# Kernel optimization log

Measured on AMD Instinct MI355X. Metric: run time of the kernel, lower is better.

Reference implementation:

```python
import jax, jax.numpy as jnp
import numpy as np

B, L, D = 4, 4096, 2048
E = 64           # num_experts
K = 2            # top_k
AUX_W = 0.01     # aux_loss_weight


def setup_inputs() -> dict:
    key = jax.random.key(0)
    kx, kw = jax.random.split(key)
    x = jax.random.normal(kx, (B, L, D), dtype=jnp.float32)
    W = jax.random.normal(kw, (E, D), dtype=jnp.float32) * 0.02  # nn.init.normal_(std=0.02)
    return {"x": x, "W": W}


def reference(x, W):
    # gate: logits [B, L, E]
    logits = jnp.einsum('bld,ed->ble', x, W)
    # full softmax over experts (used for aux loss)
    probs = jax.nn.softmax(logits, axis=-1)
    # top-k selection and renormalized weights
    top_k_logits, top_k_indices = jax.lax.top_k(logits, K)      # [B, L, K]
    top_k_weights = jax.nn.softmax(top_k_logits, axis=-1)       # [B, L, K]
    # load-balance aux loss (Switch-style): uses top-1 expert assignment
    expert_mask = jax.nn.one_hot(top_k_indices[..., 0], E, dtype=jnp.float32)  # [B, L, E]
    expert_fraction = expert_mask.mean(axis=(0, 1))              # [E]
    prob_fraction = probs.mean(axis=(0, 1))                      # [E]
    aux_loss = E * jnp.sum(expert_fraction * prob_fraction) * AUX_W
    return top_k_indices, top_k_weights, aux_loss
```

## Files before the change

### kernel.cpp

```cpp
#include <hip/hip_runtime.h>

#define D_DIM 2048
#define E_NUM 64
#define M_TOK 16384
#define BK 32
#define XS_ROW 33
#define XS_TILE (64 * XS_ROW)


__global__ __launch_bounds__(128) void init_kernel(float* __restrict__ g) {
    g[threadIdx.x] = 0.0f;
}

__global__ __launch_bounds__(256) void wt_kernel(const float* __restrict__ W,
                                                 float* __restrict__ Wt) {
    const int i4 = blockIdx.x * 256 + threadIdx.x;
    const int e  = i4 >> 9;
    const int k4 = (i4 & 511) << 2;
    const float4 v = *(const float4*)&W[e * D_DIM + k4];
    Wt[(k4 + 0) * E_NUM + e] = v.x;
    Wt[(k4 + 1) * E_NUM + e] = v.y;
    Wt[(k4 + 2) * E_NUM + e] = v.z;
    Wt[(k4 + 3) * E_NUM + e] = v.w;
}

__global__ __launch_bounds__(512, 1) void fused_kernel(
    const float* __restrict__ x, const float* __restrict__ Wt,
    float* __restrict__ out, float* __restrict__ gprob, float* __restrict__ gcnt)
{
    __shared__ float lds[4 * XS_TILE];

    const int tid  = threadIdx.x;
    const int wid  = tid >> 6;
    const int lane = tid & 63;
    const int h    = wid >> 2;
    const int eb   = (wid & 3) << 4;
    const long tok0 = (long)blockIdx.x * 64;
    const int ku = __builtin_amdgcn_readfirstlane((wid >> 2) << 10);
    const int eu = __builtin_amdgcn_readfirstlane((wid & 3) << 4);

    const int sh   = tid >> 8;
    const int ss   = tid & 255;
    const int srow = ss >> 2;
    const int sc   = (ss & 3) << 2;
    const float* xsrc = x + (tok0 + srow) * D_DIM + (sh << 10) + sc;

    double accd[16];
    #pragma unroll
    for (int e = 0; e < 16; ++e) accd[e] = 0.0;

    float4 v0 = *(const float4*)(xsrc);
    float4 v1 = *(const float4*)(xsrc + 16);
    {
        float* d = lds + (sh * 2) * XS_TILE + srow * XS_ROW + sc;
        d[0] = v0.x; d[1] = v0.y; d[2] = v0.z; d[3] = v0.w;
        d[16] = v1.x; d[17] = v1.y; d[18] = v1.z; d[19] = v1.w;
    }
    __syncthreads();

    for (int it = 0; it < 32; ++it) {
        if (it < 31) {
            const float* p = xsrc + (it + 1) * BK;
            v0 = *(const float4*)(p);
            v1 = *(const float4*)(p + 16);
        }
        const float* xb = lds + (h * 2 + (it & 1)) * XS_TILE + lane * XS_ROW;
        const int kb0 = ku + it * BK;
        #pragma unroll 1
        for (int c2 = 0; c2 < 2; ++c2) {
            float accc[16];
            #pragma unroll
            for (int e = 0; e < 16; ++e) accc[e] = 0.0f;
            const float* xc = xb + c2 * 16;
            const float* wp = Wt + (size_t)(kb0 + c2 * 16) * E_NUM + eu;
            #pragma unroll 1
            for (int q = 0; q < 4; ++q) {
                const float xr[4] = { xc[q * 4 + 0], xc[q * 4 + 1],
                                      xc[q * 4 + 2], xc[q * 4 + 3] };
                float4 w0[4], w1[4], w2[4], w3[4];
                #pragma unroll
                for (int k2 = 0; k2 < 4; ++k2) {
                    const float* wr = wp + (q * 4 + k2) * E_NUM;
                    w0[k2] = *(const float4*)(wr + 0);
                    w1[k2] = *(const float4*)(wr + 4);
                    w2[k2] = *(const float4*)(wr + 8);
                    w3[k2] = *(const float4*)(wr + 12);
                }
                #pragma unroll
                for (int k2 = 0; k2 < 4; ++k2) {
                    const float xk = xr[k2];
                    accc[0]  += xk * w0[k2].x;  accc[1]  += xk * w0[k2].y;
                    accc[2]  += xk * w0[k2].z;  accc[3]  += xk * w0[k2].w;
                    accc[4]  += xk * w1[k2].x;  accc[5]  += xk * w1[k2].y;
                    accc[6]  += xk * w1[k2].z;  accc[7]  += xk * w1[k2].w;
                    accc[8]  += xk * w2[k2].x;  accc[9]  += xk * w2[k2].y;
                    accc[10] += xk * w2[k2].z;  accc[11] += xk * w2[k2].w;
                    accc[12] += xk * w3[k2].x;  accc[13] += xk * w3[k2].y;
                    accc[14] += xk * w3[k2].z;  accc[15] += xk * w3[k2].w;
                }
            }
            #pragma unroll
            for (int e = 0; e < 16; ++e) accd[e] += (double)accc[e];
        }
        if (it < 31) {
            float* d = lds + (sh * 2 + ((it + 1) & 1)) * XS_TILE + srow * XS_ROW + sc;
            d[0] = v0.x; d[1] = v0.y; d[2] = v0.z; d[3] = v0.w;
            d[16] = v1.x; d[17] = v1.y; d[18] = v1.z; d[19] = v1.w;
        }
        __syncthreads();
    }

    {
        float* sp = lds + h * 4096 + lane * 64 + eb;
        *(float4*)(sp + 0)  = make_float4((float)accd[0],  (float)accd[1],
                                          (float)accd[2],  (float)accd[3]);
        *(float4*)(sp + 4)  = make_float4((float)accd[4],  (float)accd[5],
                                          (float)accd[6],  (float)accd[7]);
        *(float4*)(sp + 8)  = make_float4((float)accd[8],  (float)accd[9],
                                          (float)accd[10], (float)accd[11]);
        *(float4*)(sp + 12) = make_float4((float)accd[12], (float)accd[13],
                                          (float)accd[14], (float)accd[15]);
    }
    __syncthreads();

    float pacc = 0.0f, cacc = 0.0f;
    if (h == 0) {
        const int q = wid & 3;
        for (int i = 0; i < 16; ++i) {
            const int  tl = q * 16 + i;
            const long t  = tok0 + tl;
            const float l = lds[tl * 64 + lane] + lds[4096 + tl * 64 + lane];
            float m1 = l; int i1 = lane;
            #pragma unroll
            for (int off = 32; off > 0; off >>= 1) {
                const float ov = __shfl_xor(m1, off, 64);
                const int   oi = __shfl_xor(i1, off, 64);
                if (ov > m1 || (ov == m1 && oi < i1)) { m1 = ov; i1 = oi; }
            }
            const float p = __expf(l - m1);
            float s = p;
            #pragma unroll
            for (int off = 32; off > 0; off >>= 1) s += __shfl_xor(s, off, 64);
            pacc += p / s;
            if (lane == i1) cacc += 1.0f;
            const float lm = (lane == i1) ? -1e30f : l;
            float m2 = lm; int i2 = lane;
            #pragma unroll
            for (int off = 32; off > 0; off >>= 1) {
                const float ov = __shfl_xor(m2, off, 64);
                const int   oi = __shfl_xor(i2, off, 64);
                if (ov > m2 || (ov == m2 && oi < i2)) { m2 = ov; i2 = oi; }
            }
            if (lane == 0) {
                out[2 * t]     = (float)i1;
                out[2 * t + 1] = (float)i2;
                const float w1 = 1.0f / (1.0f + __expf(m2 - m1));
                out[2 * M_TOK + 2 * t]     = w1;
                out[2 * M_TOK + 2 * t + 1] = 1.0f - w1;
            }
        }
    }
    __syncthreads();
    if (h == 0) {
        lds[(wid & 3) * 64 + lane]       = pacc;
        lds[256 + (wid & 3) * 64 + lane] = cacc;
    }
    __syncthreads();
    if (wid == 0) {
        atomicAdd(&gprob[lane], lds[lane] + lds[64 + lane] + lds[128 + lane] + lds[192 + lane]);
        atomicAdd(&gcnt[lane],  lds[256 + lane] + lds[320 + lane] + lds[384 + lane] + lds[448 + lane]);
    }
}

__global__ __launch_bounds__(64) void aux_kernel(
    const float* __restrict__ gprob, const float* __restrict__ gcnt,
    float* __restrict__ out)
{
    const int lane = threadIdx.x;
    float v = gprob[lane] * gcnt[lane];
    #pragma unroll
    for (int off = 32; off > 0; off >>= 1) v += __shfl_xor(v, off, 64);
    if (lane == 0)
        out[4 * M_TOK] = 64.0f * 0.01f * v / ((float)M_TOK * (float)M_TOK);
}

extern "C" void kernel_launch(void* const* d_in, const int* in_sizes, int n_in,
                              void* d_out, int out_size, void* d_ws, size_t ws_size,
                              hipStream_t stream)
{
    const float* x = (const float*)d_in[0];
    const float* W = (const float*)d_in[1];
    float* out   = (float*)d_out;
    float* gprob = (float*)d_ws;
    float* gcnt  = gprob + 64;
    float* Wt    = gprob + 128;

    init_kernel<<<1, 128, 0, stream>>>(gprob);
    wt_kernel<<<128, 256, 0, stream>>>(W, Wt);
    fused_kernel<<<256, 512, 0, stream>>>(x, Wt, out, gprob, gcnt);
    aux_kernel<<<1, 64, 0, stream>>>(gprob, gcnt, out);
}
```

Baseline: 293.1 us.

## Double wavefronts per block, halve experts per wave, fold init into transpose kernel

Blocks grow from 512 to 1024 threads, so each wavefront accumulates 8 experts instead of 16. The x staging rows are padded to 36 so shared-memory reads and writes can use float4. This is meant to raise latency hiding and cut register pressure on the single-block-per-CU grid of 256 blocks. The zero-initialisation kernel is merged into the weight transpose kernel to save one launch. Each W row now gets loaded by twice as many waves in total, and the top-k epilogue still runs on only 4 of the 16 waves.

```diff
diff --git a/kernel.cpp b/kernel.cpp
--- a/kernel.cpp
+++ b/kernel.cpp
@@ -4,16 +4,14 @@
 #define E_NUM 64
 #define M_TOK 16384
 #define BK 32
-#define XS_ROW 33
+#define XS_ROW 36
 #define XS_TILE (64 * XS_ROW)
 
 
-__global__ __launch_bounds__(128) void init_kernel(float* __restrict__ g) {
-    g[threadIdx.x] = 0.0f;
-}
-
 __global__ __launch_bounds__(256) void wt_kernel(const float* __restrict__ W,
-                                                 float* __restrict__ Wt) {
+                                                 float* __restrict__ Wt,
+                                                 float* __restrict__ g) {
+    if (blockIdx.x == 0 && threadIdx.x < 128) g[threadIdx.x] = 0.0f;
     const int i4 = blockIdx.x * 256 + threadIdx.x;
     const int e  = i4 >> 9;
     const int k4 = (i4 & 511) << 2;
@@ -24,7 +22,7 @@
     Wt[(k4 + 3) * E_NUM + e] = v.w;
 }
 
-__global__ __launch_bounds__(512, 1) void fused_kernel(
+__global__ __launch_bounds__(1024, 1) void fused_kernel(
     const float* __restrict__ x, const float* __restrict__ Wt,
     float* __restrict__ out, float* __restrict__ gprob, float* __restrict__ gcnt)
 {
@@ -33,99 +31,79 @@
     const int tid  = threadIdx.x;
     const int wid  = tid >> 6;
     const int lane = tid & 63;
-    const int h    = wid >> 2;
-    const int eb   = (wid & 3) << 4;
+    const int h    = wid >> 3;
+    const int eb   = (wid & 7) << 3;
     const long tok0 = (long)blockIdx.x * 64;
-    const int ku = __builtin_amdgcn_readfirstlane((wid >> 2) << 10);
-    const int eu = __builtin_amdgcn_readfirstlane((wid & 3) << 4);
+    const int ku = __builtin_amdgcn_readfirstlane(h << 10);
+    const int eu = __builtin_amdgcn_readfirstlane(eb);
 
-    const int sh   = tid >> 8;
-    const int ss   = tid & 255;
-    const int srow = ss >> 2;
-    const int sc   = (ss & 3) << 2;
+    const int sh   = tid >> 9;
+    const int ss   = tid & 511;
+    const int srow = ss >> 3;
+    const int sc   = (ss & 7) << 2;
     const float* xsrc = x + (tok0 + srow) * D_DIM + (sh << 10) + sc;
 
-    double accd[16];
+    double accd[8];
     #pragma unroll
-    for (int e = 0; e < 16; ++e) accd[e] = 0.0;
+    for (int e = 0; e < 8; ++e) accd[e] = 0.0;
 
     float4 v0 = *(const float4*)(xsrc);
-    float4 v1 = *(const float4*)(xsrc + 16);
-    {
-        float* d = lds + (sh * 2) * XS_TILE + srow * XS_ROW + sc;
-        d[0] = v0.x; d[1] = v0.y; d[2] = v0.z; d[3] = v0.w;
-        d[16] = v1.x; d[17] = v1.y; d[18] = v1.z; d[19] = v1.w;
-    }
+    *(float4*)&lds[(sh * 2) * XS_TILE + srow * XS_ROW + sc] = v0;
     __syncthreads();
 
     for (int it = 0; it < 32; ++it) {
-        if (it < 31) {
-            const float* p = xsrc + (it + 1) * BK;
-            v0 = *(const float4*)(p);
-            v1 = *(const float4*)(p + 16);
-        }
+        if (it < 31) v0 = *(const float4*)(xsrc + (it + 1) * BK);
         const float* xb = lds + (h * 2 + (it & 1)) * XS_TILE + lane * XS_ROW;
         const int kb0 = ku + it * BK;
         #pragma unroll 1
         for (int c2 = 0; c2 < 2; ++c2) {
-            float accc[16];
+            float accc[8];
             #pragma unroll
-            for (int e = 0; e < 16; ++e) accc[e] = 0.0f;
+            for (int e = 0; e < 8; ++e) accc[e] = 0.0f;
             const float* xc = xb + c2 * 16;
             const float* wp = Wt + (size_t)(kb0 + c2 * 16) * E_NUM + eu;
             #pragma unroll 1
-            for (int q = 0; q < 4; ++q) {
-                const float xr[4] = { xc[q * 4 + 0], xc[q * 4 + 1],
-                                      xc[q * 4 + 2], xc[q * 4 + 3] };
-                float4 w0[4], w1[4], w2[4], w3[4];
+            for (int q = 0; q < 2; ++q) {
+                const float4 xa = *(const float4*)(xc + q * 8);
+                const float4 xs4 = *(const float4*)(xc + q * 8 + 4);
+                const float xr[8] = { xa.x, xa.y, xa.z, xa.w,
+                                      xs4.x, xs4.y, xs4.z, xs4.w };
+                float4 w0[8], w1[8];
                 #pragma unroll
-                for (int k2 = 0; k2 < 4; ++k2) {
-                    const float* wr = wp + (q * 4 + k2) * E_NUM;
+                for (int k2 = 0; k2 < 8; ++k2) {
+                    const float* wr = wp + (q * 8 + k2) * E_NUM;
                     w0[k2] = *(const float4*)(wr + 0);
                     w1[k2] = *(const float4*)(wr + 4);
-                    w2[k2] = *(const float4*)(wr + 8);
-                    w3[k2] = *(const float4*)(wr + 12);
                 }
                 #pragma unroll
-                for (int k2 = 0; k2 < 4; ++k2) {
+                for (int k2 = 0; k2 < 8; ++k2) {
                     const float xk = xr[k2];
-                    accc[0]  += xk * w0[k2].x;  accc[1]  += xk * w0[k2].y;
-                    accc[2]  += xk * w0[k2].z;  accc[3]  += xk * w0[k2].w;
-                    accc[4]  += xk * w1[k2].x;  accc[5]  += xk * w1[k2].y;
-                    accc[6]  += xk * w1[k2].z;  accc[7]  += xk * w1[k2].w;
-                    accc[8]  += xk * w2[k2].x;  accc[9]  += xk * w2[k2].y;
-                    accc[10] += xk * w2[k2].z;  accc[11] += xk * w2[k2].w;
-                    accc[12] += xk * w3[k2].x;  accc[13] += xk * w3[k2].y;
-                    accc[14] += xk * w3[k2].z;  accc[15] += xk * w3[k2].w;
+                    accc[0] += xk * w0[k2].x;  accc[1] += xk * w0[k2].y;
+                    accc[2] += xk * w0[k2].z;  accc[3] += xk * w0[k2].w;
+                    accc[4] += xk * w1[k2].x;  accc[5] += xk * w1[k2].y;
+                    accc[6] += xk * w1[k2].z;  accc[7] += xk * w1[k2].w;
                 }
             }
             #pragma unroll
-            for (int e = 0; e < 16; ++e) accd[e] += (double)accc[e];
+            for (int e = 0; e < 8; ++e) accd[e] += (double)accc[e];
         }
-        if (it < 31) {
-            float* d = lds + (sh * 2 + ((it + 1) & 1)) * XS_TILE + srow * XS_ROW + sc;
-            d[0] = v0.x; d[1] = v0.y; d[2] = v0.z; d[3] = v0.w;
-            d[16] = v1.x; d[17] = v1.y; d[18] = v1.z; d[19] = v1.w;
-        }
+        if (it < 31)
+            *(float4*)&lds[(sh * 2 + ((it + 1) & 1)) * XS_TILE + srow * XS_ROW + sc] = v0;
         __syncthreads();
     }
 
     {
         float* sp = lds + h * 4096 + lane * 64 + eb;
-        *(float4*)(sp + 0)  = make_float4((float)accd[0],  (float)accd[1],
-                                          (float)accd[2],  (float)accd[3]);
-        *(float4*)(sp + 4)  = make_float4((float)accd[4],  (float)accd[5],
-                                          (float)accd[6],  (float)accd[7]);
-        *(float4*)(sp + 8)  = make_float4((float)accd[8],  (float)accd[9],
-                                          (float)accd[10], (float)accd[11]);
-        *(float4*)(sp + 12) = make_float4((float)accd[12], (float)accd[13],
-                                          (float)accd[14], (float)accd[15]);
+        *(float4*)(sp + 0) = make_float4((float)accd[0], (float)accd[1],
+                                         (float)accd[2], (float)accd[3]);
+        *(float4*)(sp + 4) = make_float4((float)accd[4], (float)accd[5],
+                                         (float)accd[6], (float)accd[7]);
     }
     __syncthreads();
 
     float pacc = 0.0f, cacc = 0.0f;
-    if (h == 0) {
-        const int q = wid & 3;
+    if (wid < 4) {
+        const int q = wid;
         for (int i = 0; i < 16; ++i) {
             const int  tl = q * 16 + i;
             const long t  = tok0 + tl;
@@ -161,9 +139,9 @@
         }
     }
     __syncthreads();
-    if (h == 0) {
-        lds[(wid & 3) * 64 + lane]       = pacc;
-        lds[256 + (wid & 3) * 64 + lane] = cacc;
+    if (wid < 4) {
+        lds[wid * 64 + lane]       = pacc;
+        lds[256 + wid * 64 + lane] = cacc;
     }
     __syncthreads();
     if (wid == 0) {
@@ -195,8 +173,7 @@
     float* gcnt  = gprob + 64;
     float* Wt    = gprob + 128;
 
-    init_kernel<<<1, 128, 0, stream>>>(gprob);
-    wt_kernel<<<128, 256, 0, stream>>>(W, Wt);
-    fused_kernel<<<256, 512, 0, stream>>>(x, Wt, out, gprob, gcnt);
+    wt_kernel<<<128, 256, 0, stream>>>(W, Wt, gprob);
+    fused_kernel<<<256, 1024, 0, stream>>>(x, Wt, out, gprob, gcnt);
     aux_kernel<<<1, 64, 0, stream>>>(gprob, gcnt, out);
 }
```

New measurement: 280.9 us. 4.1% less time.
